# Kernel tuning notes

Measured on AMD Instinct MI355X. Metric: run time of the kernel, lower is better.

## Reference

```python
import jax, jax.numpy as jnp
import numpy as np

QMIN, QMAX = -128.0, 127.0  # int8 range


def setup_inputs() -> dict:
    key = jax.random.key(0)
    k1, k2, k3 = jax.random.split(key, 3)
    B, S, IN, OUT = 4, 2048, 4096, 4096
    x = jax.random.normal(k1, (B, S, IN), dtype=jnp.float32)
    quantized_weight = jax.random.randint(k2, (OUT, IN), -128, 128, dtype=jnp.int32)
    weight_scale = jnp.float32(0.01)
    activation_scale = jnp.float32(0.05)
    bias = jax.random.normal(k3, (OUT,), dtype=jnp.float32)
    return {
        "x": x,
        "quantized_weight": quantized_weight,
        "weight_scale": weight_scale,
        "activation_scale": activation_scale,
        "bias": bias,
    }


def reference(x, quantized_weight, weight_scale, activation_scale, bias):
    # Fake-quantize activations to int8 grid (round, clamp), then dequantize.
    x_q = jnp.clip(jnp.round(x / activation_scale), QMIN, QMAX)
    x_f = x_q * activation_scale  # [B,S,IN] fp32
    # Dequantize int8 weights.
    w_f = quantized_weight.astype(jnp.float32) * weight_scale  # [OUT,IN]
    # F.linear: x @ W^T + b
    out = jnp.einsum("bsi,oi->bso", x_f, w_f) + bias
    return out
```

## Files before the change

### kernel.cpp

```cpp
#include <hip/hip_runtime.h>


#define MD 8192
#define ND 4096
#define KD 4096
#define KT (KD / 64)

typedef int   int4v   __attribute__((ext_vector_type(4)));
typedef float float4v __attribute__((ext_vector_type(4)));


__device__ __forceinline__ unsigned int quant1(float v, float s) {
  float q = rintf(v / s);
  q = fmaxf(-128.0f, fminf(127.0f, q));
  return ((unsigned int)(int)q) & 0xffu;
}

__global__ __launch_bounds__(256) void quant_x_kernel(
    const float* __restrict__ x, const float* __restrict__ as_p,
    signed char* __restrict__ aq) {
  __shared__ unsigned int lds[4096];
  const float s = as_p[0];
  int bid = blockIdx.x;
  int r0 = (bid >> 4) * 64;
  int k0 = (bid & 15) * 256;
  int tid = threadIdx.x, lane = tid & 63, wv = tid >> 6;

  int subL = wv * 4 + (lane >> 4);
  int kgroup = (lane & 15) >> 2;
  int c = lane & 3;
  int X = subL * 4 + kgroup;
  int xm = X & 15;
  const float* src = x + (size_t)(r0 + wv * 16) * KD + k0 + lane * 4;
#pragma unroll
  for (int i = 0; i < 16; ++i) {
    float4v v = *(const float4v*)(src + (size_t)i * KD);
    unsigned int d = quant1(v.x, s) | (quant1(v.y, s) << 8) |
                     (quant1(v.z, s) << 16) | (quant1(v.w, s) << 24);
    lds[X * 64 + ((i ^ xm) << 2) + c] = d;
  }
  __syncthreads();

  size_t obase = ((size_t)(r0 >> 4) * KT + (k0 >> 6)) * 1024;
  int y = tid & 15;
#pragma unroll
  for (int a = 0; a < 4; ++a) {
    int Xr = (a * 4 + (tid >> 6)) * 4 + ((tid & 63) >> 4);
    int4v vv = *(const int4v*)((const char*)lds + Xr * 256 + ((y ^ (Xr & 15)) << 4));
    *(int4v*)(aq + obase + (size_t)a * KT * 1024 + tid * 16) = vv;
  }
}

__global__ __launch_bounds__(256) void pack_w_kernel(
    const int* __restrict__ w, signed char* __restrict__ wq) {
  __shared__ unsigned int lds[4096];
  int bid = blockIdx.x;
  int r0 = (bid >> 4) * 64;
  int k0 = (bid & 15) * 256;
  int tid = threadIdx.x, lane = tid & 63, wv = tid >> 6;

  int subL = wv * 4 + (lane >> 4);
  int kgroup = (lane & 15) >> 2;
  int c = lane & 3;
  int X = subL * 4 + kgroup;
  int xm = X & 15;
  const int* src = w + (size_t)(r0 + wv * 16) * KD + k0 + lane * 4;
#pragma unroll
  for (int i = 0; i < 16; ++i) {
    int4v v = *(const int4v*)(src + (size_t)i * KD);
    unsigned int d = (v.x & 0xff) | ((v.y & 0xff) << 8) |
                     ((v.z & 0xff) << 16) | ((v.w & 0xff) << 24);
    lds[X * 64 + ((i ^ xm) << 2) + c] = d;
  }
  __syncthreads();

  size_t obase = ((size_t)(r0 >> 4) * KT + (k0 >> 6)) * 1024;
  int y = tid & 15;
#pragma unroll
  for (int a = 0; a < 4; ++a) {
    int Xr = (a * 4 + (tid >> 6)) * 4 + ((tid & 63) >> 4);
    int4v vv = *(const int4v*)((const char*)lds + Xr * 256 + ((y ^ (Xr & 15)) << 4));
    *(int4v*)(wq + obase + (size_t)a * KT * 1024 + tid * 16) = vv;
  }
}

__global__ __launch_bounds__(256) void gemm_i8_kernel(
    const signed char* __restrict__ aq, const signed char* __restrict__ wq,
    const float* __restrict__ ws_p, const float* __restrict__ as_p,
    const float* __restrict__ bias, float* __restrict__ out) {
  __shared__ signed char lds_a[8192];
  __shared__ signed char lds_b[8192];

  int nwg = gridDim.x;
  int cpx = nwg >> 3;
  int bid = blockIdx.x;
  int wg  = (bid & 7) * cpx + (bid >> 3);
  const int NT = ND / 128;
  int tm = wg / NT;
  int tn = wg - tm * NT;

  int tid  = threadIdx.x;
  int lane = tid & 63;
  int wv   = tid >> 6;
  int wr   = wv >> 1;
  int wc   = wv & 1;

  const size_t a_base = (size_t)(tm * 8) * KT * 1024;
  const size_t b_base = (size_t)(tn * 8) * KT * 1024;

  int4v acc[4][4];
#pragma unroll
  for (int i = 0; i < 4; ++i)
#pragma unroll
    for (int j = 0; j < 4; ++j) acc[i][j] = (int4v){0, 0, 0, 0};

  for (int kt = 0; kt < KT; ++kt) {
#pragma unroll
    for (int j = 0; j < 2; ++j) {
      int ia = wv + j * 4;
      const signed char* ga = aq + a_base + ((size_t)ia * KT + kt) * 1024 + lane * 16;
      __builtin_amdgcn_global_load_lds(
          (const __attribute__((address_space(1))) void*)ga,
          (__attribute__((address_space(3))) void*)(lds_a + ia * 1024), 16, 0, 0);
      const signed char* gb = wq + b_base + ((size_t)ia * KT + kt) * 1024 + lane * 16;
      __builtin_amdgcn_global_load_lds(
          (const __attribute__((address_space(1))) void*)gb,
          (__attribute__((address_space(3))) void*)(lds_b + ia * 1024), 16, 0, 0);
    }
    __syncthreads();

    int4v afrag[4], bfrag[4];
#pragma unroll
    for (int rb = 0; rb < 4; ++rb)
      afrag[rb] = *(const int4v*)(lds_a + (wr * 4 + rb) * 1024 + lane * 16);
#pragma unroll
    for (int cb = 0; cb < 4; ++cb)
      bfrag[cb] = *(const int4v*)(lds_b + (wc * 4 + cb) * 1024 + lane * 16);

#pragma unroll
    for (int rb = 0; rb < 4; ++rb)
#pragma unroll
      for (int cb = 0; cb < 4; ++cb)
        acc[rb][cb] = __builtin_amdgcn_mfma_i32_16x16x64_i8(
            afrag[rb], bfrag[cb], acc[rb][cb], 0, 0, 0);

    __syncthreads();
  }

  float scale = ws_p[0] * as_p[0];
  int col0 = tn * 128 + wc * 64 + (lane & 15);
  int row0 = tm * 128 + wr * 64 + ((lane >> 4) << 2);
  float bv[4];
#pragma unroll
  for (int cb = 0; cb < 4; ++cb) bv[cb] = bias[col0 + cb * 16];
#pragma unroll
  for (int rb = 0; rb < 4; ++rb) {
#pragma unroll
    for (int cb = 0; cb < 4; ++cb) {
      int col = col0 + cb * 16;
#pragma unroll
      for (int j = 0; j < 4; ++j) {
        int row = row0 + rb * 16 + j;
        out[(size_t)row * ND + col] = (float)acc[rb][cb][j] * scale + bv[cb];
      }
    }
  }
}

extern "C" void kernel_launch(void* const* d_in, const int* in_sizes, int n_in,
                              void* d_out, int out_size, void* d_ws, size_t ws_size,
                              hipStream_t stream) {
  const float* x    = (const float*)d_in[0];
  const int*   qw   = (const int*)d_in[1];
  const float* wsc  = (const float*)d_in[2];
  const float* asc  = (const float*)d_in[3];
  const float* bias = (const float*)d_in[4];
  float* out = (float*)d_out;

  signed char* aq = (signed char*)d_ws;
  signed char* wq = aq + (size_t)MD * KD;

  quant_x_kernel<<<(MD / 64) * (KD / 256), 256, 0, stream>>>(x, asc, aq);
  pack_w_kernel<<<(ND / 64) * (KD / 256), 256, 0, stream>>>(qw, wq);
  gemm_i8_kernel<<<(MD / 128) * (ND / 128), 256, 0, stream>>>(aq, wq, wsc, asc, bias, out);
}
```

Baseline: 411.5 us.

## Enlarge int8 GEMM tile to 256x256 with 8 waves and double-buffered LDS

The GEMM tile grows from 128x128 to 256x256 and the block from 4 to 8 waves, each wave now computing 128x64 (8x4 MFMA tiles). A second LDS buffer lets the next k-slice be fetched with global_load_lds while the current one is consumed, leaving one barrier per iteration. The larger tile cuts global traffic per output and the prefetch aims to hide load latency. The cost is 64KB of LDS per block, which with launch_bounds(512,2) limits occupancy, plus more accumulator registers.

```diff
diff --git a/kernel.cpp b/kernel.cpp
--- a/kernel.cpp
+++ b/kernel.cpp
@@ -84,77 +84,93 @@
   }
 }
 
-__global__ __launch_bounds__(256) void gemm_i8_kernel(
+#define STAGE(buf, kt) do {                                                   \
+    _Pragma("unroll")                                                         \
+    for (int j = 0; j < 2; ++j) {                                             \
+      const signed char* ga =                                                 \
+          aq + ((size_t)(a_sub0 + j * 8 + wv) * KT + (kt)) * 1024 + lane * 16;\
+      __builtin_amdgcn_global_load_lds(                                       \
+          (const __attribute__((address_space(1))) void*)ga,                  \
+          (__attribute__((address_space(3))) void*)                           \
+              (lds_g + (buf) * 32768 + (j * 8 + wv) * 1024), 16, 0, 0);       \
+      const signed char* gb =                                                 \
+          wq + ((size_t)(b_sub0 + j * 8 + wv) * KT + (kt)) * 1024 + lane * 16;\
+      __builtin_amdgcn_global_load_lds(                                       \
+          (const __attribute__((address_space(1))) void*)gb,                  \
+          (__attribute__((address_space(3))) void*)                           \
+              (lds_g + (buf) * 32768 + 16384 + (j * 8 + wv) * 1024), 16, 0, 0);\
+    }                                                                         \
+  } while (0)
+
+__global__ __launch_bounds__(512, 2) void gemm_i8_kernel(
     const signed char* __restrict__ aq, const signed char* __restrict__ wq,
     const float* __restrict__ ws_p, const float* __restrict__ as_p,
     const float* __restrict__ bias, float* __restrict__ out) {
-  __shared__ signed char lds_a[8192];
-  __shared__ signed char lds_b[8192];
+  __shared__ signed char lds_g[65536];
 
   int nwg = gridDim.x;
   int cpx = nwg >> 3;
   int bid = blockIdx.x;
   int wg  = (bid & 7) * cpx + (bid >> 3);
-  const int NT = ND / 128;
+  const int NT = ND / 256;
   int tm = wg / NT;
   int tn = wg - tm * NT;
 
   int tid  = threadIdx.x;
   int lane = tid & 63;
   int wv   = tid >> 6;
-  int wr   = wv >> 1;
-  int wc   = wv & 1;
-
-  const size_t a_base = (size_t)(tm * 8) * KT * 1024;
-  const size_t b_base = (size_t)(tn * 8) * KT * 1024;
-
-  int4v acc[4][4];
-#pragma unroll
-  for (int i = 0; i < 4; ++i)
+  int wr   = wv >> 2;
+  int wc   = wv & 3;
+
+  const int a_sub0 = tm * 16;
+  const int b_sub0 = tn * 16;
+
+  int4v acc[8][4];
+#pragma unroll
+  for (int i = 0; i < 8; ++i)
 #pragma unroll
     for (int j = 0; j < 4; ++j) acc[i][j] = (int4v){0, 0, 0, 0};
 
+  int cur = 0;
+  STAGE(0, 0);
+  __syncthreads();
+
   for (int kt = 0; kt < KT; ++kt) {
-#pragma unroll
-    for (int j = 0; j < 2; ++j) {
-      int ia = wv + j * 4;
-      const signed char* ga = aq + a_base + ((size_t)ia * KT + kt) * 1024 + lane * 16;
-      __builtin_amdgcn_global_load_lds(
-          (const __attribute__((address_space(1))) void*)ga,
-          (__attribute__((address_space(3))) void*)(lds_a + ia * 1024), 16, 0, 0);
-      const signed char* gb = wq + b_base + ((size_t)ia * KT + kt) * 1024 + lane * 16;
-      __builtin_amdgcn_global_load_lds(
-          (const __attribute__((address_space(1))) void*)gb,
-          (__attribute__((address_space(3))) void*)(lds_b + ia * 1024), 16, 0, 0);
+    if (kt + 1 < KT) {
+      STAGE(cur ^ 1, kt + 1);
     }
-    __syncthreads();
-
-    int4v afrag[4], bfrag[4];
-#pragma unroll
-    for (int rb = 0; rb < 4; ++rb)
-      afrag[rb] = *(const int4v*)(lds_a + (wr * 4 + rb) * 1024 + lane * 16);
+    __builtin_amdgcn_sched_barrier(0);
+
+    const signed char* abuf = lds_g + cur * 32768;
+    const signed char* bbuf = abuf + 16384;
+
+    int4v afrag[8], bfrag[4];
+#pragma unroll
+    for (int rb = 0; rb < 8; ++rb)
+      afrag[rb] = *(const int4v*)(abuf + (wr * 8 + rb) * 1024 + lane * 16);
 #pragma unroll
     for (int cb = 0; cb < 4; ++cb)
-      bfrag[cb] = *(const int4v*)(lds_b + (wc * 4 + cb) * 1024 + lane * 16);
-
-#pragma unroll
-    for (int rb = 0; rb < 4; ++rb)
+      bfrag[cb] = *(const int4v*)(bbuf + (wc * 4 + cb) * 1024 + lane * 16);
+
+#pragma unroll
+    for (int rb = 0; rb < 8; ++rb)
 #pragma unroll
       for (int cb = 0; cb < 4; ++cb)
         acc[rb][cb] = __builtin_amdgcn_mfma_i32_16x16x64_i8(
             afrag[rb], bfrag[cb], acc[rb][cb], 0, 0, 0);
 
     __syncthreads();
+    cur ^= 1;
   }
 
   float scale = ws_p[0] * as_p[0];
-  int col0 = tn * 128 + wc * 64 + (lane & 15);
-  int row0 = tm * 128 + wr * 64 + ((lane >> 4) << 2);
+  int col0 = tn * 256 + wc * 64 + (lane & 15);
+  int row0 = tm * 256 + wr * 128 + ((lane >> 4) << 2);
   float bv[4];
 #pragma unroll
   for (int cb = 0; cb < 4; ++cb) bv[cb] = bias[col0 + cb * 16];
 #pragma unroll
-  for (int rb = 0; rb < 4; ++rb) {
+  for (int rb = 0; rb < 8; ++rb) {
 #pragma unroll
     for (int cb = 0; cb < 4; ++cb) {
       int col = col0 + cb * 16;
@@ -182,5 +198,5 @@
 
   quant_x_kernel<<<(MD / 64) * (KD / 256), 256, 0, stream>>>(x, asc, aq);
   pack_w_kernel<<<(ND / 64) * (KD / 256), 256, 0, stream>>>(qw, wq);
-  gemm_i8_kernel<<<(MD / 128) * (ND / 128), 256, 0, stream>>>(aq, wq, wsc, asc, bias, out);
-}
+  gemm_i8_kernel<<<(MD / 256) * (ND / 256), 512, 0, stream>>>(aq, wq, wsc, asc, bias, out);
+}
```

Result: faster. 388.7 us (-5.5%).
